# Optimization experiments

Measured on AMD Instinct MI355X. Metric: run time of the kernel, lower is better.

Reference implementation:

```python
import jax, jax.numpy as jnp
import numpy as np

B, S, HID = 2, 2048, 1024
NH = 16
DK = HID // NH


def setup_inputs() -> dict:
    key0 = jax.random.key(0)
    ks = jax.random.split(key0, 16)
    inp = {
        "query": jax.random.normal(ks[0], (B, S, HID), dtype=jnp.float32),
        "key": jax.random.normal(ks[1], (B, S, HID), dtype=jnp.float32),
        "value": jax.random.normal(ks[2], (B, S, HID), dtype=jnp.float32),
        "bias": jax.random.uniform(ks[3], (B, S), dtype=jnp.float32),
        "mask": jax.random.randint(ks[4], (B, 1, S), 0, 2, dtype=jnp.int32),
        "wq": jax.random.normal(ks[5], (HID, HID), dtype=jnp.float32) * 0.02,
        "bq": jax.random.normal(ks[6], (HID,), dtype=jnp.float32) * 0.02,
        "wk": jax.random.normal(ks[7], (HID, HID), dtype=jnp.float32) * 0.02,
        "bk": jax.random.normal(ks[8], (HID,), dtype=jnp.float32) * 0.02,
        "wv": jax.random.normal(ks[9], (HID, HID), dtype=jnp.float32) * 0.02,
        "bv": jax.random.normal(ks[10], (HID,), dtype=jnp.float32) * 0.02,
        "wo": jax.random.normal(ks[11], (HID, HID), dtype=jnp.float32) * 0.02,
        "bo": jax.random.normal(ks[12], (HID,), dtype=jnp.float32) * 0.02,
    }
    return inp


def reference(query, key, value, bias, mask, wq, bq, wk, bk, wv, bv, wo, bo):
    b, s, hid = query.shape
    # attn_bias_type == 'both': gate K and V with per-token scalar bias
    # (dropout is eval-mode identity): x + p[..., None] * x
    key = key + bias[:, :, None] * key
    value = value + bias[:, :, None] * value

    def proj(x, w, bb):
        # torch Linear: x @ W.T + b, then split heads -> [b, nh, s, dk]
        y = x @ w.T + bb
        return y.reshape(b, s, NH, DK).transpose(0, 2, 1, 3)

    q = proj(query, wq, bq)
    k = proj(key, wk, bk)
    v = proj(value, wv, bv)

    scores = jnp.einsum("bhqd,bhkd->bhqk", q, k) / jnp.sqrt(jnp.asarray(DK, q.dtype))
    m = mask[:, None]  # [b,1,1,s] broadcast over heads and query positions
    scores = jnp.where(m == 0, jnp.asarray(-10000.0, scores.dtype), scores)
    p_attn = jax.nn.softmax(scores, axis=-1)
    x = jnp.einsum("bhqk,bhkd->bhqd", p_attn, v)
    x = x.transpose(0, 2, 1, 3).reshape(b, s, hid)
    return x @ wo.T + bo
```

## Files before the change

kernel.cpp:

```cpp
#include <hip/hip_runtime.h>
#include <stdint.h>

#define NB   2
#define SS   2048
#define HIDN 1024
#define NHEAD 16
#define DKK  64

typedef __attribute__((ext_vector_type(8))) short bf16x8;
typedef __attribute__((ext_vector_type(4))) float f32x4;

__device__ __forceinline__ uint16_t f2bf(float f) {
    uint32_t u = __float_as_uint(f);
    u += 0x7FFF + ((u >> 16) & 1);
    return (uint16_t)(u >> 16);
}
__device__ __forceinline__ uint32_t pk2(float f0, float f1) {
    uint32_t u0 = __float_as_uint(f0);
    uint32_t u1 = __float_as_uint(f1);
    u0 += 0x7FFF + ((u0 >> 16) & 1);
    u1 += 0x7FFF + ((u1 >> 16) & 1);
    return (u0 >> 16) | (u1 & 0xFFFF0000u);
}
__device__ __forceinline__ uint4 pack8(const float* __restrict__ s, float sc) {
    float4 a = *(const float4*)s;
    float4 b = *(const float4*)(s + 4);
    uint4 r;
    r.x = pk2(sc * a.x, sc * a.y);
    r.y = pk2(sc * a.z, sc * a.w);
    r.z = pk2(sc * b.x, sc * b.y);
    r.w = pk2(sc * b.z, sc * b.w);
    return r;
}
__device__ __forceinline__ void gl_lds16(const uint16_t* g, uint16_t* l) {
    __builtin_amdgcn_global_load_lds((const __attribute__((address_space(1))) void*)g,
                                     (__attribute__((address_space(3))) void*)l,
                                     16, 0, 0);
}

__global__ __launch_bounds__(256, 4)
void cvt_all(const float* __restrict__ q, const float* __restrict__ k,
             const float* __restrict__ v, const float* __restrict__ bias,
             const float* __restrict__ w0, const float* __restrict__ w1,
             const float* __restrict__ w2, const float* __restrict__ w3,
             uint16_t* __restrict__ q16, uint16_t* __restrict__ k16,
             uint16_t* __restrict__ v16, uint16_t* __restrict__ w16o)
{
    int i = blockIdx.x * 256 + threadIdx.x;
    if (i < 524288) {
        size_t e = (size_t)i * 8;
        float sc = 1.0f + bias[i >> 7];
        *(uint4*)(q16 + e) = pack8(q + e, 1.0f);
        *(uint4*)(k16 + e) = pack8(k + e, sc);
        *(uint4*)(v16 + e) = pack8(v + e, sc);
    } else {
        int j = i - 524288;
        const float* src = (j < 131072) ? w0 : (j < 262144) ? w1
                         : (j < 393216) ? w2 : w3;
        size_t e = (size_t)(j & 131071) * 8;
        *(uint4*)(w16o + (size_t)(j >> 17) * 1048576 + e) = pack8(src + e, 1.0f);
    }
}

__device__ __forceinline__ void gemm_core(const uint16_t* __restrict__ A,
                                          const uint16_t* __restrict__ W,
                                          uint16_t* __restrict__ As0,
                                          uint16_t* __restrict__ As1,
                                          uint16_t* __restrict__ Bs0,
                                          uint16_t* __restrict__ Bs1,
                                          int m0, int n0,
                                          f32x4 acc[4][2])
{
    const int t    = threadIdx.x;
    const int w    = t >> 6;
    const int lane = t & 63;
    const int q    = lane >> 4;
    const int lr   = lane & 15;
    const int wr   = (w >> 1) * 64;
    const int wc   = (w & 1) * 32;
    const int srow = lane >> 3;
    const int sg   = (lane & 7) ^ srow;

#pragma unroll
    for (int c = 0; c < 4; ++c) {
        int r = w * 32 + c * 8;
        gl_lds16(A + (size_t)(m0 + r + srow) * HIDN + sg * 8, As0 + r * 64);
    }
#pragma unroll
    for (int c = 0; c < 2; ++c) {
        int r = w * 16 + c * 8;
        gl_lds16(W + (size_t)(n0 + r + srow) * HIDN + sg * 8, Bs0 + r * 64);
    }

    for (int it = 0; it < 16; ++it) {
        uint16_t* Asc = (it & 1) ? As1 : As0;
        uint16_t* Bsc = (it & 1) ? Bs1 : Bs0;
        uint16_t* Asn = (it & 1) ? As0 : As1;
        uint16_t* Bsn = (it & 1) ? Bs0 : Bs1;
        __syncthreads();
        if (it + 1 < 16) {
            int k0 = (it + 1) * 64;
#pragma unroll
            for (int c = 0; c < 4; ++c) {
                int r = w * 32 + c * 8;
                gl_lds16(A + (size_t)(m0 + r + srow) * HIDN + k0 + sg * 8,
                         Asn + r * 64);
            }
#pragma unroll
            for (int c = 0; c < 2; ++c) {
                int r = w * 16 + c * 8;
                gl_lds16(W + (size_t)(n0 + r + srow) * HIDN + k0 + sg * 8,
                         Bsn + r * 64);
            }
        }
        bf16x8 af[2][4], bfr[2][2];
#pragma unroll
        for (int s = 0; s < 2; ++s) {
#pragma unroll
            for (int i = 0; i < 4; ++i)
                af[s][i] = *(const bf16x8*)&Asc[(wr + i * 16 + lr) * 64 +
                                                (((s * 4 + q) ^ (lr & 7)) * 8)];
#pragma unroll
            for (int j = 0; j < 2; ++j)
                bfr[s][j] = *(const bf16x8*)&Bsc[(wc + j * 16 + lr) * 64 +
                                                 (((s * 4 + q) ^ (lr & 7)) * 8)];
        }
#pragma unroll
        for (int s = 0; s < 2; ++s)
#pragma unroll
            for (int i = 0; i < 4; ++i)
#pragma unroll
                for (int j = 0; j < 2; ++j)
                    acc[i][j] = __builtin_amdgcn_mfma_f32_16x16x32_bf16(
                        af[s][i], bfr[s][j], acc[i][j], 0, 0, 0);
    }
}

__global__ __launch_bounds__(256, 3)
void gemm_qkv(const uint16_t* __restrict__ Qin, const uint16_t* __restrict__ Kin,
              const uint16_t* __restrict__ Vin, const uint16_t* __restrict__ W16,
              const float* __restrict__ bq, const float* __restrict__ bk,
              const float* __restrict__ bv,
              uint16_t* __restrict__ Qb, uint16_t* __restrict__ Kb,
              uint16_t* __restrict__ Vtb)
{
    __shared__ __align__(16) uint16_t As[2][128 * 64];
    __shared__ __align__(16) uint16_t Bs[2][64 * 64];

    const int z = blockIdx.z;
    const uint16_t* A    = (z == 0) ? Qin : (z == 1) ? Kin : Vin;
    const uint16_t* W    = W16 + (size_t)z * 1048576;
    const float*    bias = (z == 0) ? bq : (z == 1) ? bk : bv;
    const float     osc  = (z == 0) ? 0.125f : 1.0f;

    const int t    = threadIdx.x;
    const int w    = t >> 6;
    const int lane = t & 63;
    const int q    = lane >> 4;
    const int lr   = lane & 15;
    const int wr   = (w >> 1) * 64;
    const int wc   = (w & 1) * 32;
    const int m0   = blockIdx.y * 128;
    const int n0   = blockIdx.x * 64;

    f32x4 acc[4][2] = {};
    gemm_core(A, W, As[0], As[1], Bs[0], Bs[1], m0, n0, acc);

    if (z < 2) {
        uint16_t* o = (z == 0) ? Qb : Kb;
#pragma unroll
        for (int i = 0; i < 4; ++i)
#pragma unroll
            for (int j = 0; j < 2; ++j) {
                int gn = n0 + wc + j * 16 + lr;
                float bvx = bias[gn];
#pragma unroll
                for (int r = 0; r < 4; ++r) {
                    int row = m0 + wr + i * 16 + q * 4 + r;
                    int b = row >> 11, s = row & 2047;
                    size_t dst = (size_t)b * (NHEAD * SS * DKK)
                               + (size_t)(gn >> 6) * (SS * DKK)
                               + (size_t)s * DKK + (gn & 63);
                    o[dst] = f2bf((acc[i][j][r] + bvx) * osc);
                }
            }
    } else {
        __syncthreads();
        uint16_t* Tr = (uint16_t*)As;
#pragma unroll
        for (int i = 0; i < 4; ++i)
#pragma unroll
            for (int j = 0; j < 2; ++j) {
                int d = wc + j * 16 + lr;
                float bvx = bias[n0 + d];
#pragma unroll
                for (int r = 0; r < 4; ++r) {
                    int sl = wr + i * 16 + q * 4 + r;
                    Tr[d * 136 + sl] = f2bf(acc[i][j][r] + bvx);
                }
            }
        __syncthreads();
        int b = m0 >> 11, h = n0 >> 6;
#pragma unroll
        for (int p = 0; p < 4; ++p) {
            int idx = p * 256 + t;
            int d   = idx >> 4;
            int sc8 = (idx & 15) * 8;
            size_t dst = ((size_t)(b * NHEAD + h) * DKK + d) * SS
                       + (m0 & 2047) + sc8;
            *(uint4*)&Vtb[dst] = *(const uint4*)&Tr[d * 136 + sc8];
        }
    }
}

__global__ __launch_bounds__(256, 3)
void gemm_out(const uint16_t* __restrict__ Xb, const uint16_t* __restrict__ W,
              const float* __restrict__ bias, float* __restrict__ out)
{
    __shared__ __align__(16) uint16_t As[2][128 * 64];
    __shared__ __align__(16) uint16_t Bs[2][64 * 64];

    const int t    = threadIdx.x;
    const int w    = t >> 6;
    const int lane = t & 63;
    const int q    = lane >> 4;
    const int lr   = lane & 15;
    const int wr   = (w >> 1) * 64;
    const int wc   = (w & 1) * 32;
    const int m0   = blockIdx.y * 128;
    const int n0   = blockIdx.x * 64;

    f32x4 acc[4][2] = {};
    gemm_core(Xb, W, As[0], As[1], Bs[0], Bs[1], m0, n0, acc);

#pragma unroll
    for (int i = 0; i < 4; ++i)
#pragma unroll
        for (int j = 0; j < 2; ++j) {
            int gn = n0 + wc + j * 16 + lr;
            float bvx = bias[gn];
#pragma unroll
            for (int r = 0; r < 4; ++r) {
                int row = m0 + wr + i * 16 + q * 4 + r;
                out[(size_t)row * HIDN + gn] = acc[i][j][r] + bvx;
            }
        }
}

__global__ __launch_bounds__(512, 4)
void flash_attn(const uint16_t* __restrict__ Qg, const uint16_t* __restrict__ Kg,
                const uint16_t* __restrict__ Vtg, const int* __restrict__ mask,
                uint16_t* __restrict__ X)
{
    __shared__ __align__(16) uint16_t QP[128 * 72];
    __shared__ __align__(16) uint16_t Ks[64 * 72];
    __shared__ __align__(16) uint16_t Vs[64 * 72];
    __shared__ __align__(16) float Amf[SS];

    const int t    = threadIdx.x;
    const int w    = t >> 6;
    const int lane = t & 63;
    const int q    = lane >> 4;
    const int lr   = lane & 15;
    const int bh   = blockIdx.y;
    const int b    = bh >> 4;
    const int h    = bh & 15;
    const int q0   = blockIdx.x * 128;
    const size_t head = (size_t)bh * SS * DKK;

#pragma unroll
    for (int p = 0; p < 2; ++p) {
        int idx = p * 512 + t;
        int row = idx >> 3;
        int col = (idx & 7) * 8;
        *(uint4*)&QP[row * 72 + col] =
            *(const uint4*)(Qg + head + (size_t)(q0 + row) * DKK + col);
    }
#pragma unroll
    for (int p = 0; p < 4; ++p) {
        int i = p * 512 + t;
        Amf[i] = (mask[b * SS + i] == 0) ? -10000.0f : 0.0f;
    }
    __syncthreads();

    bf16x8 qf[2];
#pragma unroll
    for (int s = 0; s < 2; ++s)
        qf[s] = *(const bf16x8*)&QP[(w * 16 + lr) * 72 + s * 32 + q * 8];

    float mst = -1e30f, lst = 0.0f;
    f32x4 oacc[4] = {};

    for (int kv0 = 0; kv0 < SS; kv0 += 64) {
        {
            int row = t >> 3;
            int col = (t & 7) * 8;
            *(uint4*)&Ks[row * 72 + col] =
                *(const uint4*)(Kg + head + (size_t)(kv0 + row) * DKK + col);
            *(uint4*)&Vs[row * 72 + col] =
                *(const uint4*)(Vtg + head + (size_t)row * SS + kv0 + col);
        }
        __syncthreads();

        f32x4 st[4];
#pragma unroll
        for (int ni = 0; ni < 4; ++ni) {
            bf16x8 kf0 = *(const bf16x8*)&Ks[(ni * 16 + lr) * 72 + 0  + q * 8];
            bf16x8 kf1 = *(const bf16x8*)&Ks[(ni * 16 + lr) * 72 + 32 + q * 8];
            f32x4 z = {0.0f, 0.0f, 0.0f, 0.0f};
            z = __builtin_amdgcn_mfma_f32_16x16x32_bf16(kf0, qf[0], z, 0, 0, 0);
            z = __builtin_amdgcn_mfma_f32_16x16x32_bf16(kf1, qf[1], z, 0, 0, 0);
            st[ni] = z;
        }

        float rmax = -1e30f;
#pragma unroll
        for (int ni = 0; ni < 4; ++ni) {
            float4 am = *(const float4*)&Amf[kv0 + ni * 16 + q * 4];
            st[ni][0] += am.x; st[ni][1] += am.y;
            st[ni][2] += am.z; st[ni][3] += am.w;
#pragma unroll
            for (int r = 0; r < 4; ++r) rmax = fmaxf(rmax, st[ni][r]);
        }
        rmax = fmaxf(rmax, __shfl_xor(rmax, 16));
        rmax = fmaxf(rmax, __shfl_xor(rmax, 32));

        float mnew  = fmaxf(mst, rmax);
        float alpha = __expf(mst - mnew);
        mst = mnew;

        float rsum = 0.0f;
#pragma unroll
        for (int ni = 0; ni < 4; ++ni) {
            float p0 = __expf(st[ni][0] - mst);
            float p1 = __expf(st[ni][1] - mst);
            float p2 = __expf(st[ni][2] - mst);
            float p3 = __expf(st[ni][3] - mst);
            rsum += (p0 + p1) + (p2 + p3);
            uint2 pw = make_uint2(pk2(p0, p1), pk2(p2, p3));
            *(uint2*)&QP[(w * 16 + lr) * 72 + ni * 16 + q * 4] = pw;
        }
        rsum += __shfl_xor(rsum, 16);
        rsum += __shfl_xor(rsum, 32);
        lst = lst * alpha + rsum;
#pragma unroll
        for (int dj = 0; dj < 4; ++dj) {
            oacc[dj][0] *= alpha; oacc[dj][1] *= alpha;
            oacc[dj][2] *= alpha; oacc[dj][3] *= alpha;
        }

#pragma unroll
        for (int ks = 0; ks < 2; ++ks) {
            bf16x8 pfB = *(const bf16x8*)&QP[(w * 16 + lr) * 72 + ks * 32 + q * 8];
#pragma unroll
            for (int dj = 0; dj < 4; ++dj) {
                bf16x8 vfA = *(const bf16x8*)&Vs[(dj * 16 + lr) * 72 + ks * 32 + q * 8];
                oacc[dj] = __builtin_amdgcn_mfma_f32_16x16x32_bf16(vfA, pfB, oacc[dj], 0, 0, 0);
            }
        }
        __syncthreads();
    }

    {
        float inv = 1.0f / lst;
        int s = q0 + w * 16 + lr;
        uint16_t* xp = X + (size_t)(b * SS + s) * HIDN + h * DKK;
#pragma unroll
        for (int dj = 0; dj < 4; ++dj) {
            uint2 pw = make_uint2(pk2(oacc[dj][0] * inv, oacc[dj][1] * inv),
                                  pk2(oacc[dj][2] * inv, oacc[dj][3] * inv));
            *(uint2*)(xp + dj * 16 + q * 4) = pw;
        }
    }
}

extern "C" void kernel_launch(void* const* d_in, const int* in_sizes, int n_in,
                              void* d_out, int out_size, void* d_ws, size_t ws_size,
                              hipStream_t stream) {
    const float* query = (const float*)d_in[0];
    const float* key   = (const float*)d_in[1];
    const float* value = (const float*)d_in[2];
    const float* bias  = (const float*)d_in[3];
    const int*   mask  = (const int*)d_in[4];
    const float* wq = (const float*)d_in[5];
    const float* bq = (const float*)d_in[6];
    const float* wk = (const float*)d_in[7];
    const float* bk = (const float*)d_in[8];
    const float* wv = (const float*)d_in[9];
    const float* bv = (const float*)d_in[10];
    const float* wo = (const float*)d_in[11];
    const float* bo = (const float*)d_in[12];

    const size_t TEN = (size_t)NB * SS * HIDN;
    uint16_t* Qin = (uint16_t*)d_ws;
    uint16_t* Kin = Qin + TEN;
    uint16_t* Vin = Kin + TEN;
    uint16_t* W16 = Vin + TEN;
    uint16_t* Qb  = W16 + 4 * 1048576;
    uint16_t* Kb  = Qb + TEN;
    uint16_t* Vtb = Kb + TEN;
    uint16_t* Xb  = Qin;

    cvt_all<<<4096, 256, 0, stream>>>(query, key, value, bias,
                                      wq, wk, wv, wo, Qin, Kin, Vin, W16);
    gemm_qkv<<<dim3(16, 32, 3), 256, 0, stream>>>(Qin, Kin, Vin, W16,
                                                  bq, bk, bv, Qb, Kb, Vtb);
    flash_attn<<<dim3(SS / 128, NB * NHEAD), 512, 0, stream>>>(Qb, Kb, Vtb, mask, Xb);
    gemm_out<<<dim3(16, 32), 256, 0, stream>>>(Xb, W16 + 3 * 1048576, bo, (float*)d_out);
}
```

Measured before the change: 256.5 us.

## Enlarge GEMM tiles to 128x128 and give each flash-attention wave 32 query rows

The shared GEMM core now computes a 128x128 output tile with K-step 32 (16 MFMAs per wave per step) in place of 128x64 with K-step 64. It also drops the XOR swizzle on LDS, which risks bank conflicts. The V-transpose epilogue now runs in two halves over the wider tile. Flash attention moves to 256 threads, with each wave processing two 16-row query blocks, so K/V fragments loaded from LDS are reused across both, and the mask load is vectorised. Together these aim to raise arithmetic intensity per LDS and global load, at the cost of more registers and fewer blocks.

```diff
diff --git a/kernel.cpp b/kernel.cpp
--- a/kernel.cpp
+++ b/kernel.cpp
@@ -64,12 +64,9 @@
 
 __device__ __forceinline__ void gemm_core(const uint16_t* __restrict__ A,
                                           const uint16_t* __restrict__ W,
-                                          uint16_t* __restrict__ As0,
-                                          uint16_t* __restrict__ As1,
-                                          uint16_t* __restrict__ Bs0,
-                                          uint16_t* __restrict__ Bs1,
+                                          uint16_t (*__restrict__ SM)[8192],
                                           int m0, int n0,
-                                          f32x4 acc[4][2])
+                                          f32x4 acc[4][4])
 {
     const int t    = threadIdx.x;
     const int w    = t >> 6;
@@ -77,62 +74,45 @@
     const int q    = lane >> 4;
     const int lr   = lane & 15;
     const int wr   = (w >> 1) * 64;
-    const int wc   = (w & 1) * 32;
-    const int srow = lane >> 3;
-    const int sg   = (lane & 7) ^ srow;
-
-#pragma unroll
-    for (int c = 0; c < 4; ++c) {
-        int r = w * 32 + c * 8;
-        gl_lds16(A + (size_t)(m0 + r + srow) * HIDN + sg * 8, As0 + r * 64);
-    }
-#pragma unroll
-    for (int c = 0; c < 2; ++c) {
-        int r = w * 16 + c * 8;
-        gl_lds16(W + (size_t)(n0 + r + srow) * HIDN + sg * 8, Bs0 + r * 64);
-    }
-
-    for (int it = 0; it < 16; ++it) {
-        uint16_t* Asc = (it & 1) ? As1 : As0;
-        uint16_t* Bsc = (it & 1) ? Bs1 : Bs0;
-        uint16_t* Asn = (it & 1) ? As0 : As1;
-        uint16_t* Bsn = (it & 1) ? Bs0 : Bs1;
+    const int wc   = (w & 1) * 64;
+    const int rsub = lane >> 2;
+    const int cg   = (lane & 3) * 8;
+
+#pragma unroll
+    for (int p = 0; p < 2; ++p) {
+        int rb = p * 64 + w * 16;
+        gl_lds16(A + (size_t)(m0 + rb + rsub) * HIDN + cg, &SM[0][rb * 32]);
+        gl_lds16(W + (size_t)(n0 + rb + rsub) * HIDN + cg, &SM[0][4096 + rb * 32]);
+    }
+
+    for (int it = 0; it < 32; ++it) {
+        uint16_t* cur = SM[it & 1];
+        uint16_t* nxt = SM[(it & 1) ^ 1];
         __syncthreads();
-        if (it + 1 < 16) {
-            int k0 = (it + 1) * 64;
-#pragma unroll
-            for (int c = 0; c < 4; ++c) {
-                int r = w * 32 + c * 8;
-                gl_lds16(A + (size_t)(m0 + r + srow) * HIDN + k0 + sg * 8,
-                         Asn + r * 64);
-            }
-#pragma unroll
-            for (int c = 0; c < 2; ++c) {
-                int r = w * 16 + c * 8;
-                gl_lds16(W + (size_t)(n0 + r + srow) * HIDN + k0 + sg * 8,
-                         Bsn + r * 64);
-            }
-        }
-        bf16x8 af[2][4], bfr[2][2];
-#pragma unroll
-        for (int s = 0; s < 2; ++s) {
-#pragma unroll
-            for (int i = 0; i < 4; ++i)
-                af[s][i] = *(const bf16x8*)&Asc[(wr + i * 16 + lr) * 64 +
-                                                (((s * 4 + q) ^ (lr & 7)) * 8)];
-#pragma unroll
-            for (int j = 0; j < 2; ++j)
-                bfr[s][j] = *(const bf16x8*)&Bsc[(wc + j * 16 + lr) * 64 +
-                                                 (((s * 4 + q) ^ (lr & 7)) * 8)];
-        }
-#pragma unroll
-        for (int s = 0; s < 2; ++s)
-#pragma unroll
-            for (int i = 0; i < 4; ++i)
-#pragma unroll
-                for (int j = 0; j < 2; ++j)
-                    acc[i][j] = __builtin_amdgcn_mfma_f32_16x16x32_bf16(
-                        af[s][i], bfr[s][j], acc[i][j], 0, 0, 0);
+        if (it + 1 < 32) {
+            int k0 = (it + 1) * 32;
+#pragma unroll
+            for (int p = 0; p < 2; ++p) {
+                int rb = p * 64 + w * 16;
+                gl_lds16(A + (size_t)(m0 + rb + rsub) * HIDN + k0 + cg,
+                         &nxt[rb * 32]);
+                gl_lds16(W + (size_t)(n0 + rb + rsub) * HIDN + k0 + cg,
+                         &nxt[4096 + rb * 32]);
+            }
+        }
+        bf16x8 af[4], bf[4];
+#pragma unroll
+        for (int i = 0; i < 4; ++i)
+            af[i] = *(const bf16x8*)&cur[(wr + i * 16 + lr) * 32 + q * 8];
+#pragma unroll
+        for (int j = 0; j < 4; ++j)
+            bf[j] = *(const bf16x8*)&cur[4096 + (wc + j * 16 + lr) * 32 + q * 8];
+#pragma unroll
+        for (int i = 0; i < 4; ++i)
+#pragma unroll
+            for (int j = 0; j < 4; ++j)
+                acc[i][j] = __builtin_amdgcn_mfma_f32_16x16x32_bf16(
+                    af[i], bf[j], acc[i][j], 0, 0, 0);
     }
 }
 
@@ -144,8 +124,7 @@
               uint16_t* __restrict__ Qb, uint16_t* __restrict__ Kb,
               uint16_t* __restrict__ Vtb)
 {
-    __shared__ __align__(16) uint16_t As[2][128 * 64];
-    __shared__ __align__(16) uint16_t Bs[2][64 * 64];
+    __shared__ __align__(16) uint16_t SM[2][8192];
 
     const int z = blockIdx.z;
     const uint16_t* A    = (z == 0) ? Qin : (z == 1) ? Kin : Vin;
@@ -159,19 +138,19 @@
     const int q    = lane >> 4;
     const int lr   = lane & 15;
     const int wr   = (w >> 1) * 64;
-    const int wc   = (w & 1) * 32;
+    const int wc   = (w & 1) * 64;
     const int m0   = blockIdx.y * 128;
-    const int n0   = blockIdx.x * 64;
-
-    f32x4 acc[4][2] = {};
-    gemm_core(A, W, As[0], As[1], Bs[0], Bs[1], m0, n0, acc);
+    const int n0   = blockIdx.x * 128;
+
+    f32x4 acc[4][4] = {};
+    gemm_core(A, W, SM, m0, n0, acc);
 
     if (z < 2) {
         uint16_t* o = (z == 0) ? Qb : Kb;
 #pragma unroll
         for (int i = 0; i < 4; ++i)
 #pragma unroll
-            for (int j = 0; j < 2; ++j) {
+            for (int j = 0; j < 4; ++j) {
                 int gn = n0 + wc + j * 16 + lr;
                 float bvx = bias[gn];
 #pragma unroll
@@ -185,30 +164,34 @@
                 }
             }
     } else {
-        __syncthreads();
-        uint16_t* Tr = (uint16_t*)As;
-#pragma unroll
-        for (int i = 0; i < 4; ++i)
-#pragma unroll
-            for (int j = 0; j < 2; ++j) {
-                int d = wc + j * 16 + lr;
-                float bvx = bias[n0 + d];
-#pragma unroll
-                for (int r = 0; r < 4; ++r) {
-                    int sl = wr + i * 16 + q * 4 + r;
-                    Tr[d * 136 + sl] = f2bf(acc[i][j][r] + bvx);
+        uint16_t* Tr = &SM[0][0];
+        int bb = m0 >> 11, hb = n0 >> 6;
+#pragma unroll
+        for (int dh = 0; dh < 2; ++dh) {
+            __syncthreads();
+            if ((w & 1) == dh) {
+#pragma unroll
+                for (int j = 0; j < 4; ++j) {
+                    int dl = j * 16 + lr;
+                    float bvx = bias[n0 + dh * 64 + dl];
+#pragma unroll
+                    for (int i = 0; i < 4; ++i)
+#pragma unroll
+                        for (int r = 0; r < 4; ++r)
+                            Tr[dl * 136 + wr + i * 16 + q * 4 + r] =
+                                f2bf(acc[i][j][r] + bvx);
                 }
             }
-        __syncthreads();
-        int b = m0 >> 11, h = n0 >> 6;
-#pragma unroll
-        for (int p = 0; p < 4; ++p) {
-            int idx = p * 256 + t;
-            int d   = idx >> 4;
-            int sc8 = (idx & 15) * 8;
-            size_t dst = ((size_t)(b * NHEAD + h) * DKK + d) * SS
-                       + (m0 & 2047) + sc8;
-            *(uint4*)&Vtb[dst] = *(const uint4*)&Tr[d * 136 + sc8];
+            __syncthreads();
+#pragma unroll
+            for (int p = 0; p < 4; ++p) {
+                int idx = p * 256 + t;
+                int d   = idx >> 4;
+                int sc8 = (idx & 15) * 8;
+                size_t dst = ((size_t)(bb * NHEAD + hb + dh) * DKK + d) * SS
+                           + (m0 & 2047) + sc8;
+                *(uint4*)&Vtb[dst] = *(const uint4*)&Tr[d * 136 + sc8];
+            }
         }
     }
 }
@@ -217,8 +200,7 @@
 void gemm_out(const uint16_t* __restrict__ Xb, const uint16_t* __restrict__ W,
               const float* __restrict__ bias, float* __restrict__ out)
 {
-    __shared__ __align__(16) uint16_t As[2][128 * 64];
-    __shared__ __align__(16) uint16_t Bs[2][64 * 64];
+    __shared__ __align__(16) uint16_t SM[2][8192];
 
     const int t    = threadIdx.x;
     const int w    = t >> 6;
@@ -226,17 +208,17 @@
     const int q    = lane >> 4;
     const int lr   = lane & 15;
     const int wr   = (w >> 1) * 64;
-    const int wc   = (w & 1) * 32;
+    const int wc   = (w & 1) * 64;
     const int m0   = blockIdx.y * 128;
-    const int n0   = blockIdx.x * 64;
-
-    f32x4 acc[4][2] = {};
-    gemm_core(Xb, W, As[0], As[1], Bs[0], Bs[1], m0, n0, acc);
+    const int n0   = blockIdx.x * 128;
+
+    f32x4 acc[4][4] = {};
+    gemm_core(Xb, W, SM, m0, n0, acc);
 
 #pragma unroll
     for (int i = 0; i < 4; ++i)
 #pragma unroll
-        for (int j = 0; j < 2; ++j) {
+        for (int j = 0; j < 4; ++j) {
             int gn = n0 + wc + j * 16 + lr;
             float bvx = bias[gn];
 #pragma unroll
@@ -247,7 +229,7 @@
         }
 }
 
-__global__ __launch_bounds__(512, 4)
+__global__ __launch_bounds__(256, 3)
 void flash_attn(const uint16_t* __restrict__ Qg, const uint16_t* __restrict__ Kg,
                 const uint16_t* __restrict__ Vtg, const int* __restrict__ mask,
                 uint16_t* __restrict__ X)
@@ -269,32 +251,45 @@
     const size_t head = (size_t)bh * SS * DKK;
 
 #pragma unroll
-    for (int p = 0; p < 2; ++p) {
-        int idx = p * 512 + t;
+    for (int p = 0; p < 4; ++p) {
+        int idx = p * 256 + t;
         int row = idx >> 3;
         int col = (idx & 7) * 8;
         *(uint4*)&QP[row * 72 + col] =
             *(const uint4*)(Qg + head + (size_t)(q0 + row) * DKK + col);
     }
-#pragma unroll
-    for (int p = 0; p < 4; ++p) {
-        int i = p * 512 + t;
-        Amf[i] = (mask[b * SS + i] == 0) ? -10000.0f : 0.0f;
+    {
+        const int4* mp = (const int4*)(mask + b * SS);
+#pragma unroll
+        for (int p = 0; p < 2; ++p) {
+            int4 m4 = mp[p * 256 + t];
+            float4 f;
+            f.x = m4.x ? 0.0f : -10000.0f;
+            f.y = m4.y ? 0.0f : -10000.0f;
+            f.z = m4.z ? 0.0f : -10000.0f;
+            f.w = m4.w ? 0.0f : -10000.0f;
+            ((float4*)Amf)[p * 256 + t] = f;
+        }
     }
     __syncthreads();
 
-    bf16x8 qf[2];
-#pragma unroll
-    for (int s = 0; s < 2; ++s)
-        qf[s] = *(const bf16x8*)&QP[(w * 16 + lr) * 72 + s * 32 + q * 8];
-
-    float mst = -1e30f, lst = 0.0f;
-    f32x4 oacc[4] = {};
+    bf16x8 qf[2][2];
+#pragma unroll
+    for (int mi = 0; mi < 2; ++mi)
+#pragma unroll
+        for (int s = 0; s < 2; ++s)
+            qf[mi][s] = *(const bf16x8*)&QP[(w * 32 + mi * 16 + lr) * 72 +
+                                            s * 32 + q * 8];
+
+    float mst[2] = {-1e30f, -1e30f}, lst[2] = {0.0f, 0.0f};
+    f32x4 oacc[2][4] = {};
 
     for (int kv0 = 0; kv0 < SS; kv0 += 64) {
-        {
-            int row = t >> 3;
-            int col = (t & 7) * 8;
+#pragma unroll
+        for (int p = 0; p < 2; ++p) {
+            int idx = p * 256 + t;
+            int row = idx >> 3;
+            int col = (idx & 7) * 8;
             *(uint4*)&Ks[row * 72 + col] =
                 *(const uint4*)(Kg + head + (size_t)(kv0 + row) * DKK + col);
             *(uint4*)&Vs[row * 72 + col] =
@@ -302,73 +297,98 @@
         }
         __syncthreads();
 
-        f32x4 st[4];
+        f32x4 st[2][4];
 #pragma unroll
         for (int ni = 0; ni < 4; ++ni) {
             bf16x8 kf0 = *(const bf16x8*)&Ks[(ni * 16 + lr) * 72 + 0  + q * 8];
             bf16x8 kf1 = *(const bf16x8*)&Ks[(ni * 16 + lr) * 72 + 32 + q * 8];
-            f32x4 z = {0.0f, 0.0f, 0.0f, 0.0f};
-            z = __builtin_amdgcn_mfma_f32_16x16x32_bf16(kf0, qf[0], z, 0, 0, 0);
-            z = __builtin_amdgcn_mfma_f32_16x16x32_bf16(kf1, qf[1], z, 0, 0, 0);
-            st[ni] = z;
-        }
-
-        float rmax = -1e30f;
+#pragma unroll
+            for (int mi = 0; mi < 2; ++mi) {
+                f32x4 z = {0.0f, 0.0f, 0.0f, 0.0f};
+                z = __builtin_amdgcn_mfma_f32_16x16x32_bf16(kf0, qf[mi][0], z, 0, 0, 0);
+                z = __builtin_amdgcn_mfma_f32_16x16x32_bf16(kf1, qf[mi][1], z, 0, 0, 0);
+                st[mi][ni] = z;
+            }
+        }
+
+        float rmax[2] = {-1e30f, -1e30f};
 #pragma unroll
         for (int ni = 0; ni < 4; ++ni) {
             float4 am = *(const float4*)&Amf[kv0 + ni * 16 + q * 4];
-            st[ni][0] += am.x; st[ni][1] += am.y;
-            st[ni][2] += am.z; st[ni][3] += am.w;
-#pragma unroll
-            for (int r = 0; r < 4; ++r) rmax = fmaxf(rmax, st[ni][r]);
-        }
-        rmax = fmaxf(rmax, __shfl_xor(rmax, 16));
-        rmax = fmaxf(rmax, __shfl_xor(rmax, 32));
-
-        float mnew  = fmaxf(mst, rmax);
-        float alpha = __expf(mst - mnew);
-        mst = mnew;
-
-        float rsum = 0.0f;
-#pragma unroll
-        for (int ni = 0; ni < 4; ++ni) {
-            float p0 = __expf(st[ni][0] - mst);
-            float p1 = __expf(st[ni][1] - mst);
-            float p2 = __expf(st[ni][2] - mst);
-            float p3 = __expf(st[ni][3] - mst);
-            rsum += (p0 + p1) + (p2 + p3);
-            uint2 pw = make_uint2(pk2(p0, p1), pk2(p2, p3));
-            *(uint2*)&QP[(w * 16 + lr) * 72 + ni * 16 + q * 4] = pw;
-        }
-        rsum += __shfl_xor(rsum, 16);
-        rsum += __shfl_xor(rsum, 32);
-        lst = lst * alpha + rsum;
+#pragma unroll
+            for (int mi = 0; mi < 2; ++mi) {
+                st[mi][ni][0] += am.x; st[mi][ni][1] += am.y;
+                st[mi][ni][2] += am.z; st[mi][ni][3] += am.w;
+#pragma unroll
+                for (int r = 0; r < 4; ++r)
+                    rmax[mi] = fmaxf(rmax[mi], st[mi][ni][r]);
+            }
+        }
+        float alpha[2], rsum[2];
+#pragma unroll
+        for (int mi = 0; mi < 2; ++mi) {
+            float v = rmax[mi];
+            v = fmaxf(v, __shfl_xor(v, 16));
+            v = fmaxf(v, __shfl_xor(v, 32));
+            float mnew = fmaxf(mst[mi], v);
+            alpha[mi] = __expf(mst[mi] - mnew);
+            mst[mi] = mnew;
+            rsum[mi] = 0.0f;
+        }
+#pragma unroll
+        for (int ni = 0; ni < 4; ++ni)
+#pragma unroll
+            for (int mi = 0; mi < 2; ++mi) {
+                float p0 = __expf(st[mi][ni][0] - mst[mi]);
+                float p1 = __expf(st[mi][ni][1] - mst[mi]);
+                float p2 = __expf(st[mi][ni][2] - mst[mi]);
+                float p3 = __expf(st[mi][ni][3] - mst[mi]);
+                rsum[mi] += (p0 + p1) + (p2 + p3);
+                uint2 pw = make_uint2(pk2(p0, p1), pk2(p2, p3));
+                *(uint2*)&QP[(w * 32 + mi * 16 + lr) * 72 + ni * 16 + q * 4] = pw;
+            }
+#pragma unroll
+        for (int mi = 0; mi < 2; ++mi) {
+            float v = rsum[mi];
+            v += __shfl_xor(v, 16);
+            v += __shfl_xor(v, 32);
+            lst[mi] = lst[mi] * alpha[mi] + v;
+#pragma unroll
+            for (int dj = 0; dj < 4; ++dj) {
+                oacc[mi][dj][0] *= alpha[mi]; oacc[mi][dj][1] *= alpha[mi];
+                oacc[mi][dj][2] *= alpha[mi]; oacc[mi][dj][3] *= alpha[mi];
+            }
+        }
+
+#pragma unroll
+        for (int ks = 0; ks < 2; ++ks) {
+            bf16x8 pfB[2];
+#pragma unroll
+            for (int mi = 0; mi < 2; ++mi)
+                pfB[mi] = *(const bf16x8*)&QP[(w * 32 + mi * 16 + lr) * 72 +
+                                              ks * 32 + q * 8];
+#pragma unroll
+            for (int dj = 0; dj < 4; ++dj) {
+                bf16x8 vfA = *(const bf16x8*)&Vs[(dj * 16 + lr) * 72 +
+                                                 ks * 32 + q * 8];
+#pragma unroll
+                for (int mi = 0; mi < 2; ++mi)
+                    oacc[mi][dj] = __builtin_amdgcn_mfma_f32_16x16x32_bf16(
+                        vfA, pfB[mi], oacc[mi][dj], 0, 0, 0);
+            }
+        }
+        __syncthreads();
+    }
+
+#pragma unroll
+    for (int mi = 0; mi < 2; ++mi) {
+        float inv = 1.0f / lst[mi];
+        int s = q0 + w * 32 + mi * 16 + lr;
+        uint16_t* xp = X + (size_t)(b * SS + s) * HIDN + h * DKK;
 #pragma unroll
         for (int dj = 0; dj < 4; ++dj) {
-            oacc[dj][0] *= alpha; oacc[dj][1] *= alpha;
-            oacc[dj][2] *= alpha; oacc[dj][3] *= alpha;
-        }
-
-#pragma unroll
-        for (int ks = 0; ks < 2; ++ks) {
-            bf16x8 pfB = *(const bf16x8*)&QP[(w * 16 + lr) * 72 + ks * 32 + q * 8];
-#pragma unroll
-            for (int dj = 0; dj < 4; ++dj) {
-                bf16x8 vfA = *(const bf16x8*)&Vs[(dj * 16 + lr) * 72 + ks * 32 + q * 8];
-                oacc[dj] = __builtin_amdgcn_mfma_f32_16x16x32_bf16(vfA, pfB, oacc[dj], 0, 0, 0);
-            }
-        }
-        __syncthreads();
-    }
-
-    {
-        float inv = 1.0f / lst;
-        int s = q0 + w * 16 + lr;
-        uint16_t* xp = X + (size_t)(b * SS + s) * HIDN + h * DKK;
-#pragma unroll
-        for (int dj = 0; dj < 4; ++dj) {
-            uint2 pw = make_uint2(pk2(oacc[dj][0] * inv, oacc[dj][1] * inv),
-                                  pk2(oacc[dj][2] * inv, oacc[dj][3] * inv));
+            uint2 pw = make_uint2(pk2(oacc[mi][dj][0] * inv, oacc[mi][dj][1] * inv),
+                                  pk2(oacc[mi][dj][2] * inv, oacc[mi][dj][3] * inv));
             *(uint2*)(xp + dj * 16 + q * 4) = pw;
         }
     }
@@ -403,8 +423,9 @@
 
     cvt_all<<<4096, 256, 0, stream>>>(query, key, value, bias,
                                       wq, wk, wv, wo, Qin, Kin, Vin, W16);
-    gemm_qkv<<<dim3(16, 32, 3), 256, 0, stream>>>(Qin, Kin, Vin, W16,
-                                                  bq, bk, bv, Qb, Kb, Vtb);
-    flash_attn<<<dim3(SS / 128, NB * NHEAD), 512, 0, stream>>>(Qb, Kb, Vtb, mask, Xb);
-    gemm_out<<<dim3(16, 32), 256, 0, stream>>>(Xb, W16 + 3 * 1048576, bo, (float*)d_out);
-}
+    gemm_qkv<<<dim3(8, 32, 3), 256, 0, stream>>>(Qin, Kin, Vin, W16,
+                                                 bq, bk, bv, Qb, Kb, Vtb);
+    flash_attn<<<dim3(16, 32), 256, 0, stream>>>(Qb, Kb, Vtb, mask, Xb);
+    gemm_out<<<dim3(8, 32), 256, 0, stream>>>(Xb, W16 + 3 * 1048576, bo,
+                                              (float*)d_out);
+}
```

Result: slower. 271.5 us (+5.9%).
